# Performance work log

Measured on AMD Instinct MI355X. Metric: run time of the kernel, lower is better.

Reference implementation:

```python
import jax, jax.numpy as jnp
import numpy as np

B, IN, OUT, H = 32768, 512, 512, 8
DH = OUT // H
SCALE = float(np.sqrt(DH))


def setup_inputs() -> dict:
    key = jax.random.key(0)
    ks = jax.random.split(key, 10)
    inp = {
        "protein_features": jax.random.normal(ks[0], (B, IN), jnp.float32),
        "ligand_features": jax.random.normal(ks[1], (B, IN), jnp.float32),
    }
    names = ["q1", "k1", "v1", "q2", "k2", "v2", "o1", "o2"]
    for i, n in enumerate(names):
        fan_in = IN if n[0] in "qkv" else OUT
        kw, kb = jax.random.split(ks[2 + i])
        inp[f"W{n}"] = jax.random.normal(kw, (OUT, fan_in), jnp.float32) * 0.02
        inp[f"b{n}"] = jax.random.normal(kb, (OUT,), jnp.float32) * 0.02
    return inp


def _attend(q, k, v):
    # q,k,v: [B, 1, H, DH]. Original code does matmul(q, k.transpose(-2,-1))
    # WITHOUT moving heads to a batch axis, so attention mixes the H heads
    # of each sample: scores [B, 1, H, H], softmax over last axis.
    scores = jnp.einsum('bshd,bsed->bshe', q, k) / SCALE
    attn = jax.nn.softmax(scores, axis=-1)
    return jnp.einsum('bshe,bsed->bshd', attn, v)  # [B,1,H,DH]


def reference(protein_features, ligand_features,
              Wq1, bq1, Wk1, bk1, Wv1, bv1,
              Wq2, bq2, Wk2, bk2, Wv2, bv2,
              Wo1, bo1, Wo2, bo2):
    Bn = protein_features.shape[0]

    def proj(x, W, b):  # torch Linear: x @ W^T + b, then view(B, -1, H, DH)
        return (x @ W.T + b).reshape(Bn, -1, H, DH)

    q1 = proj(protein_features, Wq1, bq1)
    k1 = proj(ligand_features, Wk1, bk1)
    v1 = proj(ligand_features, Wv1, bv1)
    q2 = proj(ligand_features, Wq2, bq2)
    k2 = proj(protein_features, Wk2, bk2)
    v2 = proj(protein_features, Wv2, bv2)

    out1 = _attend(q1, k1, v1).reshape(Bn, -1)  # [B, OUT]
    out2 = _attend(q2, k2, v2).reshape(Bn, -1)  # [B, OUT]
    protein_output = out1 @ Wo1.T + bo1
    ligand_output = out2 @ Wo2.T + bo2
    return (protein_output, ligand_output)
```

## Files before the change

kernel.cpp:

```cpp
#include <hip/hip_runtime.h>
#include <hip/hip_bf16.h>

#define B_ROWS 32768
#define K_DIM  512
#define NP     1536

typedef __attribute__((ext_vector_type(8))) short          bf16x8;
typedef __attribute__((ext_vector_type(8))) unsigned short u16x8;
typedef __attribute__((ext_vector_type(4))) unsigned short u16x4;
typedef __attribute__((ext_vector_type(4))) float          f32x4;

static __device__ __forceinline__ unsigned short f2bf(float f) {
  __hip_bfloat16 h = __float2bfloat16(f);
  unsigned short u; __builtin_memcpy(&u, &h, 2); return u;
}
static __device__ __forceinline__ float bf2f(unsigned short u) {
  unsigned int x = ((unsigned int)u) << 16; float f; __builtin_memcpy(&f, &x, 4); return f;
}

static __device__ __forceinline__ void gload_lds16(const void* g, void* l) {
  __builtin_amdgcn_global_load_lds(
      (const __attribute__((address_space(1))) void*)g,
      (__attribute__((address_space(3))) void*)l, 16, 0, 0);
}

__global__ __launch_bounds__(256) void pack_kernel(
    const float* __restrict__ Wq1, const float* __restrict__ Wk1,
    const float* __restrict__ Wv1, const float* __restrict__ Wq2,
    const float* __restrict__ Wk2, const float* __restrict__ Wv2,
    const float* __restrict__ Wo1, const float* __restrict__ Wo2,
    const float* __restrict__ bq1, const float* __restrict__ bk1,
    const float* __restrict__ bv1, const float* __restrict__ bq2,
    const float* __restrict__ bk2, const float* __restrict__ bv2,
    unsigned short* __restrict__ Wp, unsigned short* __restrict__ Wl,
    unsigned short* __restrict__ Wo1b, unsigned short* __restrict__ Wo2b,
    float* __restrict__ bp, float* __restrict__ bl)
{
  const int gid = blockIdx.x * 256 + threadIdx.x;
  const int idx = gid * 4;
  const float* src; unsigned short* dst;
  if (idx < 786432) {
    int n = idx >> 9, k = idx & 511;
    const float* W = (n < 512) ? (Wq1 + (size_t)n * 512)
                   : (n < 1024) ? (Wk2 + (size_t)(n - 512) * 512)
                                : (Wv2 + (size_t)(n - 1024) * 512);
    src = W + k; dst = Wp + idx;
  } else if (idx < 1572864) {
    int r = idx - 786432; int n = r >> 9, k = r & 511;
    const float* W = (n < 512) ? (Wk1 + (size_t)n * 512)
                   : (n < 1024) ? (Wv1 + (size_t)(n - 512) * 512)
                                : (Wq2 + (size_t)(n - 1024) * 512);
    src = W + k; dst = Wl + r;
  } else if (idx < 1835008) {
    int r = idx - 1572864; src = Wo1 + r; dst = Wo1b + r;
  } else {
    int r = idx - 1835008; src = Wo2 + r; dst = Wo2b + r;
  }
  float4 v = *reinterpret_cast<const float4*>(src);
  u16x4 o; o[0] = f2bf(v.x); o[1] = f2bf(v.y); o[2] = f2bf(v.z); o[3] = f2bf(v.w);
  *reinterpret_cast<u16x4*>(dst) = o;

  if (gid < 1536) {
    int n = gid;
    bp[n] = (n < 512) ? bq1[n] : (n < 1024) ? bk2[n - 512] : bv2[n - 1024];
  } else if (gid < 3072) {
    int n = gid - 1536;
    bl[n] = (n < 512) ? bk1[n] : (n < 1024) ? bv1[n - 512] : bq2[n - 1024];
  }
}

__global__ __launch_bounds__(256) void cvt_kernel(
    const float* __restrict__ xp, const float* __restrict__ xl,
    unsigned short* __restrict__ xpb, unsigned short* __restrict__ xlb)
{
  const size_t gid = (size_t)blockIdx.x * 256 + threadIdx.x;
  size_t i = gid * 8;
  const float* src; unsigned short* dst;
  if (i < 16777216) { src = xp + i; dst = xpb + i; }
  else              { src = xl + (i - 16777216); dst = xlb + (i - 16777216); }
  float4 a = ((const float4*)src)[0];
  float4 b = ((const float4*)src)[1];
  u16x8 o;
  o[0] = f2bf(a.x); o[1] = f2bf(a.y); o[2] = f2bf(a.z); o[3] = f2bf(a.w);
  o[4] = f2bf(b.x); o[5] = f2bf(b.y); o[6] = f2bf(b.z); o[7] = f2bf(b.w);
  *(u16x8*)dst = o;
}

template<bool OUT_F32>
__global__ __launch_bounds__(512, 2)
void gemm8p(const unsigned short* __restrict__ Aptr, int lda,
            const unsigned short* __restrict__ Wb,
            const float* __restrict__ bias,
            void* __restrict__ Cptr, int ldc, int ntiles)
{
  extern __shared__ __align__(16) unsigned short lds[];
  const int SLOT = 24576, BOFF = 16384;

  const int nwg = gridDim.x, cpx = nwg >> 3, b0 = blockIdx.x;
  const int wk = (b0 & 7) * cpx + (b0 >> 3);
  const int mt = wk / ntiles, nt = wk - mt * ntiles;
  const int m0 = mt << 8, n0 = nt << 7;

  const int tid = threadIdx.x;
  const int lane = tid & 63, w = tid >> 6;
  const int wm = w >> 1, wn = w & 1;
  const int fr = lane & 15, fk = lane >> 4, frx = fr & 7;

  const int r8 = tid >> 3;
  const int k8 = (tid & 7) ^ (r8 & 7);
  const unsigned short* Ab = Aptr + (size_t)(m0 + r8) * lda + k8 * 8;
  const unsigned short* Bb = Wb  + (size_t)(n0 + r8) * 512 + k8 * 8;
  const int ldsW = w * 512;

  const int koff0 = ((0 + fk) ^ frx) * 8;
  const int koff1 = ((4 + fk) ^ frx) * 8;

  f32x4 acc[4][4] = {};

#define STAGE_A(kt, s, j) \
  gload_lds16(Ab + (size_t)(kt) * 64 + (size_t)(j) * 64 * lda, \
              &lds[(s) * SLOT + (j) * 4096 + ldsW])
#define STAGE_B(kt, s, j) \
  gload_lds16(Bb + (size_t)(kt) * 64 + (size_t)(j) * 64 * 512, \
              &lds[(s) * SLOT + BOFF + (j) * 4096 + ldsW])

  STAGE_A(0, 0, 0); STAGE_A(0, 0, 1); STAGE_A(0, 0, 2); STAGE_A(0, 0, 3);
  STAGE_B(0, 0, 0); STAGE_B(0, 0, 1);
  STAGE_A(1, 1, 0); STAGE_A(1, 1, 1); STAGE_A(1, 1, 2); STAGE_A(1, 1, 3);
  STAGE_B(1, 1, 0); STAGE_B(1, 1, 1);
  asm volatile("s_waitcnt vmcnt(6)" ::: "memory");
  __builtin_amdgcn_s_barrier();

  int rd = 0;
  for (int t = 0; t < 8; ++t) {
    const int As_ = rd * SLOT, Bs_ = rd * SLOT + BOFF;
    const int st  = rd ? rd - 1 : 2;
    const bool pre = (t < 6);

    bf16x8 bfr[4][2], afq[2][2];
#pragma unroll
    for (int ni = 0; ni < 4; ++ni) {
      const int rb = Bs_ + (wn * 64 + ni * 16 + fr) * 64;
      bfr[ni][0] = *(const bf16x8*)&lds[rb + koff0];
      bfr[ni][1] = *(const bf16x8*)&lds[rb + koff1];
    }
#pragma unroll
    for (int m2 = 0; m2 < 2; ++m2) {
      const int ra = As_ + (wm * 64 + m2 * 16 + fr) * 64;
      afq[m2][0] = *(const bf16x8*)&lds[ra + koff0];
      afq[m2][1] = *(const bf16x8*)&lds[ra + koff1];
    }
    if (pre) { STAGE_A(t + 2, st, 0); STAGE_A(t + 2, st, 1); STAGE_A(t + 2, st, 2); }
    asm volatile("s_waitcnt lgkmcnt(8)" ::: "memory");
    __builtin_amdgcn_s_barrier();
    asm volatile("s_waitcnt lgkmcnt(0)" ::: "memory");
    __builtin_amdgcn_sched_barrier(0);
    __builtin_amdgcn_s_setprio(1);
#pragma unroll
    for (int m2 = 0; m2 < 2; ++m2)
#pragma unroll
      for (int ni = 0; ni < 4; ++ni)
#pragma unroll
        for (int kc = 0; kc < 2; ++kc)
          acc[m2][ni] = __builtin_amdgcn_mfma_f32_16x16x32_bf16(
              afq[m2][kc], bfr[ni][kc], acc[m2][ni], 0, 0, 0);
    __builtin_amdgcn_s_setprio(0);
    __builtin_amdgcn_s_barrier();

#pragma unroll
    for (int m2 = 0; m2 < 2; ++m2) {
      const int ra = As_ + (wm * 64 + 32 + m2 * 16 + fr) * 64;
      afq[m2][0] = *(const bf16x8*)&lds[ra + koff0];
      afq[m2][1] = *(const bf16x8*)&lds[ra + koff1];
    }
    if (pre) { STAGE_A(t + 2, st, 3); STAGE_B(t + 2, st, 0); STAGE_B(t + 2, st, 1); }
    if (pre)            asm volatile("s_waitcnt vmcnt(6)" ::: "memory");
    else if (t == 6)    asm volatile("s_waitcnt vmcnt(0)" ::: "memory");
    __builtin_amdgcn_s_barrier();
    asm volatile("s_waitcnt lgkmcnt(0)" ::: "memory");
    __builtin_amdgcn_sched_barrier(0);
    __builtin_amdgcn_s_setprio(1);
#pragma unroll
    for (int m2 = 0; m2 < 2; ++m2)
#pragma unroll
      for (int ni = 0; ni < 4; ++ni)
#pragma unroll
        for (int kc = 0; kc < 2; ++kc)
          acc[2 + m2][ni] = __builtin_amdgcn_mfma_f32_16x16x32_bf16(
              afq[m2][kc], bfr[ni][kc], acc[2 + m2][ni], 0, 0, 0);
    __builtin_amdgcn_s_setprio(0);
    __builtin_amdgcn_s_barrier();

    rd = (rd + 1 == 3) ? 0 : rd + 1;
  }
#undef STAGE_A
#undef STAGE_B

#pragma unroll
  for (int ni = 0; ni < 4; ++ni) {
    const int col = n0 + wn * 64 + ni * 16 + fr;
    const float bv = bias[col];
#pragma unroll
    for (int mi = 0; mi < 4; ++mi) {
      const int rbase = m0 + wm * 64 + mi * 16 + fk * 4;
#pragma unroll
      for (int j = 0; j < 4; ++j) {
        const float v = acc[mi][ni][j] + bv;
        if (OUT_F32)
          ((float*)Cptr)[(size_t)(rbase + j) * ldc + col] = v;
        else
          ((unsigned short*)Cptr)[(size_t)(rbase + j) * ldc + col] = f2bf(v);
      }
    }
  }
}

__global__ __launch_bounds__(256, 4)
void attn_kernel(unsigned short* __restrict__ qkvp, unsigned short* __restrict__ qkvl)
{
  __shared__ float lds[4][1696];
  const int w = threadIdx.x >> 6, lane = threadIdx.x & 63;
  const size_t r = (size_t)blockIdx.x * 4 + w;
  unsigned short* rp = qkvp + r * NP;
  unsigned short* rl = qkvl + r * NP;
  const int l8 = lane * 8;

  u16x8 q1 = *(const u16x8*)(rp + l8);
  u16x8 k2 = *(const u16x8*)(rp + 512 + l8);
  u16x8 v2 = *(const u16x8*)(rp + 1024 + l8);
  u16x8 k1 = *(const u16x8*)(rl + l8);
  u16x8 v1 = *(const u16x8*)(rl + 512 + l8);
  u16x8 q2 = *(const u16x8*)(rl + 1024 + l8);

  float* Q   = &lds[w][0];
  float* Kk  = Q + 544;
  float* V   = Kk + 544;
  float* ATT = V + 544;
  const int h = lane >> 3, e = lane & 7;
  const int sb = h * 68 + (lane & 7) * 8;

  auto stage = [&](u16x8 qv, u16x8 kv, u16x8 vv) {
#pragma unroll
    for (int j = 0; j < 8; ++j) {
      Q [sb + j] = bf2f((unsigned short)qv[j]);
      Kk[sb + j] = bf2f((unsigned short)kv[j]);
      V [sb + j] = bf2f((unsigned short)vv[j]);
    }
  };
  auto attend = [&](unsigned short* outp) {
    float s = 0.f;
#pragma unroll
    for (int d = 0; d < 64; ++d) s += Q[h * 68 + d] * Kk[e * 68 + d];
    s *= 0.125f;
    float m = fmaxf(s, __shfl_xor(s, 1, 8));
    m = fmaxf(m, __shfl_xor(m, 2, 8));
    m = fmaxf(m, __shfl_xor(m, 4, 8));
    const float p = __expf(s - m);
    float su = p;
    su += __shfl_xor(su, 1, 8); su += __shfl_xor(su, 2, 8); su += __shfl_xor(su, 4, 8);
    ATT[lane] = p / su;
    float o[8];
    const int d0 = (lane & 7) * 8;
#pragma unroll
    for (int j = 0; j < 8; ++j) {
      float a = 0.f;
#pragma unroll
      for (int e2 = 0; e2 < 8; ++e2) a += ATT[h * 8 + e2] * V[e2 * 68 + d0 + j];
      o[j] = a;
    }
    u16x8 ob;
#pragma unroll
    for (int j = 0; j < 8; ++j) ob[j] = f2bf(o[j]);
    *(u16x8*)(outp + l8) = ob;
  };

  stage(q1, k1, v1);
  attend(rp);
  stage(q2, k2, v2);
  attend(rl);
}

extern "C" void kernel_launch(void* const* d_in, const int* in_sizes, int n_in,
                              void* d_out, int out_size, void* d_ws, size_t ws_size,
                              hipStream_t stream)
{
  const float* xp  = (const float*)d_in[0];
  const float* xl  = (const float*)d_in[1];
  const float* Wq1 = (const float*)d_in[2];   const float* bq1 = (const float*)d_in[3];
  const float* Wk1 = (const float*)d_in[4];   const float* bk1 = (const float*)d_in[5];
  const float* Wv1 = (const float*)d_in[6];   const float* bv1 = (const float*)d_in[7];
  const float* Wq2 = (const float*)d_in[8];   const float* bq2 = (const float*)d_in[9];
  const float* Wk2 = (const float*)d_in[10];  const float* bk2 = (const float*)d_in[11];
  const float* Wv2 = (const float*)d_in[12];  const float* bv2 = (const float*)d_in[13];
  const float* Wo1 = (const float*)d_in[14];  const float* bo1 = (const float*)d_in[15];
  const float* Wo2 = (const float*)d_in[16];  const float* bo2 = (const float*)d_in[17];

  char* p = (char*)d_ws;
  unsigned short* Wp   = (unsigned short*)p; p += (size_t)786432 * 2;
  unsigned short* Wl   = (unsigned short*)p; p += (size_t)786432 * 2;
  unsigned short* Wo1b = (unsigned short*)p; p += (size_t)262144 * 2;
  unsigned short* Wo2b = (unsigned short*)p; p += (size_t)262144 * 2;
  float*          bp   = (float*)p;          p += (size_t)1536 * 4;
  float*          bl   = (float*)p;          p += (size_t)1536 * 4;
  unsigned short* qkvp = (unsigned short*)p; p += (size_t)B_ROWS * NP * 2;
  unsigned short* qkvl = (unsigned short*)p; p += (size_t)B_ROWS * NP * 2;
  (void)ws_size; (void)in_sizes; (void)n_in; (void)out_size;

  unsigned short* xpb = (unsigned short*)d_out;
  unsigned short* xlb = xpb + (size_t)B_ROWS * 512;

  const int LDSB = 147456;
  hipFuncSetAttribute((const void*)gemm8p<false>,
                      hipFuncAttributeMaxDynamicSharedMemorySize, LDSB);
  hipFuncSetAttribute((const void*)gemm8p<true>,
                      hipFuncAttributeMaxDynamicSharedMemorySize, LDSB);

  pack_kernel<<<2048, 256, 0, stream>>>(Wq1, Wk1, Wv1, Wq2, Wk2, Wv2, Wo1, Wo2,
                                        bq1, bk1, bv1, bq2, bk2, bv2,
                                        Wp, Wl, Wo1b, Wo2b, bp, bl);
  cvt_kernel<<<16384, 256, 0, stream>>>(xp, xl, xpb, xlb);

  gemm8p<false><<<1536, 512, LDSB, stream>>>(xpb, 512, Wp, bp, qkvp, NP, 12);
  gemm8p<false><<<1536, 512, LDSB, stream>>>(xlb, 512, Wl, bl, qkvl, NP, 12);

  attn_kernel<<<8192, 256, 0, stream>>>(qkvp, qkvl);

  float* out_p = (float*)d_out;
  float* out_l = out_p + (size_t)B_ROWS * 512;
  gemm8p<true><<<512, 512, LDSB, stream>>>(qkvp, NP, Wo1b, bo1, out_p, 512, 4);
  gemm8p<true><<<512, 512, LDSB, stream>>>(qkvl, NP, Wo2b, bo2, out_l, 512, 4);
}
```

Baseline: 502.5 us.

## Enlarge GEMM tile to 256x256 with double-buffered LDS pipeline

Widens each GEMM workgroup's output tile from 256x128 to 256x256, with 8 waves in a 2x4 layout, each computing 128x64. The three-slot, two-ahead prefetch is replaced by a two-buffer, one-ahead scheme, and grid sizes are halved to match. The goal is more reuse per LDS load and fewer redundant global reads of A. The cost is twice the accumulator registers, shallower prefetch that may expose latency, and fewer workgroups (768 and 256) to fill the CUs.

```diff
diff --git a/kernel.cpp b/kernel.cpp
--- a/kernel.cpp
+++ b/kernel.cpp
@@ -94,17 +94,17 @@
             void* __restrict__ Cptr, int ldc, int ntiles)
 {
   extern __shared__ __align__(16) unsigned short lds[];
-  const int SLOT = 24576, BOFF = 16384;
+  const int BUF = 32768, BOFF = 16384;
 
   const int nwg = gridDim.x, cpx = nwg >> 3, b0 = blockIdx.x;
   const int wk = (b0 & 7) * cpx + (b0 >> 3);
   const int mt = wk / ntiles, nt = wk - mt * ntiles;
-  const int m0 = mt << 8, n0 = nt << 7;
+  const int m0 = mt << 8, n0 = nt << 8;
 
   const int tid = threadIdx.x;
   const int lane = tid & 63, w = tid >> 6;
-  const int wm = w >> 1, wn = w & 1;
-  const int fr = lane & 15, fk = lane >> 4, frx = fr & 7;
+  const int wm = w >> 2, wn = w & 3;
+  const int fr = lane & 15, fk = lane >> 4;
 
   const int r8 = tid >> 3;
   const int k8 = (tid & 7) ^ (r8 & 7);
@@ -112,106 +112,116 @@
   const unsigned short* Bb = Wb  + (size_t)(n0 + r8) * 512 + k8 * 8;
   const int ldsW = w * 512;
 
-  const int koff0 = ((0 + fk) ^ frx) * 8;
-  const int koff1 = ((4 + fk) ^ frx) * 8;
-
-  f32x4 acc[4][4] = {};
-
-#define STAGE_A(kt, s, j) \
-  gload_lds16(Ab + (size_t)(kt) * 64 + (size_t)(j) * 64 * lda, \
-              &lds[(s) * SLOT + (j) * 4096 + ldsW])
-#define STAGE_B(kt, s, j) \
-  gload_lds16(Bb + (size_t)(kt) * 64 + (size_t)(j) * 64 * 512, \
-              &lds[(s) * SLOT + BOFF + (j) * 4096 + ldsW])
-
-  STAGE_A(0, 0, 0); STAGE_A(0, 0, 1); STAGE_A(0, 0, 2); STAGE_A(0, 0, 3);
+  const int koff0 = ((0 + fk) ^ (fr & 7)) * 8;
+  const int koff1 = ((4 + fk) ^ (fr & 7)) * 8;
+
+  f32x4 acc[8][4] = {};
+
+#define STAGE_A(kt, bf, hf) do { \
+    gload_lds16(Ab + (size_t)((hf) * 128) * lda + (kt) * 64, \
+                &lds[(bf) * BUF + ((hf) * 128) * 64 + ldsW]); \
+    gload_lds16(Ab + (size_t)((hf) * 128 + 64) * lda + (kt) * 64, \
+                &lds[(bf) * BUF + ((hf) * 128 + 64) * 64 + ldsW]); } while (0)
+#define STAGE_B(kt, bf, hf) do { \
+    gload_lds16(Bb + (size_t)((hf) * 128) * 512 + (kt) * 64, \
+                &lds[(bf) * BUF + BOFF + ((hf) * 128) * 64 + ldsW]); \
+    gload_lds16(Bb + (size_t)((hf) * 128 + 64) * 512 + (kt) * 64, \
+                &lds[(bf) * BUF + BOFF + ((hf) * 128 + 64) * 64 + ldsW]); } while (0)
+
+#define MFMA16(base) \
+  _Pragma("unroll") \
+  for (int mi = 0; mi < 4; ++mi) \
+    _Pragma("unroll") \
+    for (int ni = 0; ni < 4; ++ni) \
+      acc[(base) + mi][ni] = __builtin_amdgcn_mfma_f32_16x16x32_bf16( \
+          af[mi], bq[ni], acc[(base) + mi][ni], 0, 0, 0)
+
+  STAGE_A(0, 0, 0); STAGE_A(0, 0, 1);
   STAGE_B(0, 0, 0); STAGE_B(0, 0, 1);
-  STAGE_A(1, 1, 0); STAGE_A(1, 1, 1); STAGE_A(1, 1, 2); STAGE_A(1, 1, 3);
-  STAGE_B(1, 1, 0); STAGE_B(1, 1, 1);
-  asm volatile("s_waitcnt vmcnt(6)" ::: "memory");
+  asm volatile("s_waitcnt vmcnt(0)" ::: "memory");
   __builtin_amdgcn_s_barrier();
 
-  int rd = 0;
   for (int t = 0; t < 8; ++t) {
-    const int As_ = rd * SLOT, Bs_ = rd * SLOT + BOFF;
-    const int st  = rd ? rd - 1 : 2;
-    const bool pre = (t < 6);
-
-    bf16x8 bfr[4][2], afq[2][2];
-#pragma unroll
-    for (int ni = 0; ni < 4; ++ni) {
-      const int rb = Bs_ + (wn * 64 + ni * 16 + fr) * 64;
-      bfr[ni][0] = *(const bf16x8*)&lds[rb + koff0];
-      bfr[ni][1] = *(const bf16x8*)&lds[rb + koff1];
-    }
-#pragma unroll
-    for (int m2 = 0; m2 < 2; ++m2) {
-      const int ra = As_ + (wm * 64 + m2 * 16 + fr) * 64;
-      afq[m2][0] = *(const bf16x8*)&lds[ra + koff0];
-      afq[m2][1] = *(const bf16x8*)&lds[ra + koff1];
-    }
-    if (pre) { STAGE_A(t + 2, st, 0); STAGE_A(t + 2, st, 1); STAGE_A(t + 2, st, 2); }
-    asm volatile("s_waitcnt lgkmcnt(8)" ::: "memory");
+    const int R = t & 1, W = 1 - R;
+    const int Ard = R * BUF, Brd = R * BUF + BOFF;
+    const bool pre = (t < 7);
+    bf16x8 bq[4], af[4];
+
+#pragma unroll
+    for (int ni = 0; ni < 4; ++ni)
+      bq[ni] = *(const bf16x8*)&lds[Brd + (wn * 64 + ni * 16 + fr) * 64 + koff0];
+#pragma unroll
+    for (int mi = 0; mi < 4; ++mi)
+      af[mi] = *(const bf16x8*)&lds[Ard + (wm * 128 + mi * 16 + fr) * 64 + koff0];
+    if (pre) { STAGE_A(t + 1, W, 0); STAGE_A(t + 1, W, 1); }
     __builtin_amdgcn_s_barrier();
     asm volatile("s_waitcnt lgkmcnt(0)" ::: "memory");
     __builtin_amdgcn_sched_barrier(0);
     __builtin_amdgcn_s_setprio(1);
-#pragma unroll
-    for (int m2 = 0; m2 < 2; ++m2)
-#pragma unroll
-      for (int ni = 0; ni < 4; ++ni)
-#pragma unroll
-        for (int kc = 0; kc < 2; ++kc)
-          acc[m2][ni] = __builtin_amdgcn_mfma_f32_16x16x32_bf16(
-              afq[m2][kc], bfr[ni][kc], acc[m2][ni], 0, 0, 0);
+    MFMA16(0);
     __builtin_amdgcn_s_setprio(0);
     __builtin_amdgcn_s_barrier();
 
 #pragma unroll
-    for (int m2 = 0; m2 < 2; ++m2) {
-      const int ra = As_ + (wm * 64 + 32 + m2 * 16 + fr) * 64;
-      afq[m2][0] = *(const bf16x8*)&lds[ra + koff0];
-      afq[m2][1] = *(const bf16x8*)&lds[ra + koff1];
-    }
-    if (pre) { STAGE_A(t + 2, st, 3); STAGE_B(t + 2, st, 0); STAGE_B(t + 2, st, 1); }
-    if (pre)            asm volatile("s_waitcnt vmcnt(6)" ::: "memory");
-    else if (t == 6)    asm volatile("s_waitcnt vmcnt(0)" ::: "memory");
+    for (int mi = 0; mi < 4; ++mi)
+      af[mi] = *(const bf16x8*)&lds[Ard + (wm * 128 + 64 + mi * 16 + fr) * 64 + koff0];
+    if (pre) { STAGE_B(t + 1, W, 0); STAGE_B(t + 1, W, 1); }
     __builtin_amdgcn_s_barrier();
     asm volatile("s_waitcnt lgkmcnt(0)" ::: "memory");
     __builtin_amdgcn_sched_barrier(0);
     __builtin_amdgcn_s_setprio(1);
-#pragma unroll
-    for (int m2 = 0; m2 < 2; ++m2)
-#pragma unroll
-      for (int ni = 0; ni < 4; ++ni)
-#pragma unroll
-        for (int kc = 0; kc < 2; ++kc)
-          acc[2 + m2][ni] = __builtin_amdgcn_mfma_f32_16x16x32_bf16(
-              afq[m2][kc], bfr[ni][kc], acc[2 + m2][ni], 0, 0, 0);
+    MFMA16(4);
     __builtin_amdgcn_s_setprio(0);
     __builtin_amdgcn_s_barrier();
 
-    rd = (rd + 1 == 3) ? 0 : rd + 1;
+#pragma unroll
+    for (int ni = 0; ni < 4; ++ni)
+      bq[ni] = *(const bf16x8*)&lds[Brd + (wn * 64 + ni * 16 + fr) * 64 + koff1];
+#pragma unroll
+    for (int mi = 0; mi < 4; ++mi)
+      af[mi] = *(const bf16x8*)&lds[Ard + (wm * 128 + mi * 16 + fr) * 64 + koff1];
+    __builtin_amdgcn_s_barrier();
+    asm volatile("s_waitcnt lgkmcnt(0)" ::: "memory");
+    __builtin_amdgcn_sched_barrier(0);
+    __builtin_amdgcn_s_setprio(1);
+    MFMA16(0);
+    __builtin_amdgcn_s_setprio(0);
+    __builtin_amdgcn_s_barrier();
+
+#pragma unroll
+    for (int mi = 0; mi < 4; ++mi)
+      af[mi] = *(const bf16x8*)&lds[Ard + (wm * 128 + 64 + mi * 16 + fr) * 64 + koff1];
+    if (pre) asm volatile("s_waitcnt vmcnt(0)" ::: "memory");
+    __builtin_amdgcn_s_barrier();
+    asm volatile("s_waitcnt lgkmcnt(0)" ::: "memory");
+    __builtin_amdgcn_sched_barrier(0);
+    __builtin_amdgcn_s_setprio(1);
+    MFMA16(4);
+    __builtin_amdgcn_s_setprio(0);
+    __builtin_amdgcn_s_barrier();
   }
 #undef STAGE_A
 #undef STAGE_B
+#undef MFMA16
 
 #pragma unroll
   for (int ni = 0; ni < 4; ++ni) {
     const int col = n0 + wn * 64 + ni * 16 + fr;
     const float bv = bias[col];
 #pragma unroll
-    for (int mi = 0; mi < 4; ++mi) {
-      const int rbase = m0 + wm * 64 + mi * 16 + fk * 4;
-#pragma unroll
-      for (int j = 0; j < 4; ++j) {
-        const float v = acc[mi][ni][j] + bv;
-        if (OUT_F32)
-          ((float*)Cptr)[(size_t)(rbase + j) * ldc + col] = v;
-        else
-          ((unsigned short*)Cptr)[(size_t)(rbase + j) * ldc + col] = f2bf(v);
+    for (int mh = 0; mh < 2; ++mh)
+#pragma unroll
+      for (int mi = 0; mi < 4; ++mi) {
+        const int rbase = m0 + wm * 128 + mh * 64 + mi * 16 + fk * 4;
+#pragma unroll
+        for (int j = 0; j < 4; ++j) {
+          const float v = acc[mh * 4 + mi][ni][j] + bv;
+          if (OUT_F32)
+            ((float*)Cptr)[(size_t)(rbase + j) * ldc + col] = v;
+          else
+            ((unsigned short*)Cptr)[(size_t)(rbase + j) * ldc + col] = f2bf(v);
+        }
       }
-    }
   }
 }
 
@@ -309,7 +319,7 @@
   unsigned short* xpb = (unsigned short*)d_out;
   unsigned short* xlb = xpb + (size_t)B_ROWS * 512;
 
-  const int LDSB = 147456;
+  const int LDSB = 131072;
   hipFuncSetAttribute((const void*)gemm8p<false>,
                       hipFuncAttributeMaxDynamicSharedMemorySize, LDSB);
   hipFuncSetAttribute((const void*)gemm8p<true>,
@@ -320,13 +330,13 @@
                                         Wp, Wl, Wo1b, Wo2b, bp, bl);
   cvt_kernel<<<16384, 256, 0, stream>>>(xp, xl, xpb, xlb);
 
-  gemm8p<false><<<1536, 512, LDSB, stream>>>(xpb, 512, Wp, bp, qkvp, NP, 12);
-  gemm8p<false><<<1536, 512, LDSB, stream>>>(xlb, 512, Wl, bl, qkvl, NP, 12);
+  gemm8p<false><<<768, 512, LDSB, stream>>>(xpb, 512, Wp, bp, qkvp, NP, 6);
+  gemm8p<false><<<768, 512, LDSB, stream>>>(xlb, 512, Wl, bl, qkvl, NP, 6);
 
   attn_kernel<<<8192, 256, 0, stream>>>(qkvp, qkvl);
 
   float* out_p = (float*)d_out;
   float* out_l = out_p + (size_t)B_ROWS * 512;
-  gemm8p<true><<<512, 512, LDSB, stream>>>(qkvp, NP, Wo1b, bo1, out_p, 512, 4);
-  gemm8p<true><<<512, 512, LDSB, stream>>>(qkvl, NP, Wo2b, bo2, out_l, 512, 4);
-}
+  gemm8p<true><<<256, 512, LDSB, stream>>>(qkvp, NP, Wo1b, bo1, out_p, 512, 2);
+  gemm8p<true><<<256, 512, LDSB, stream>>>(qkvl, NP, Wo2b, bo2, out_l, 512, 2);
+}
```

New measurement: 537.5 us. +7.0%, slower.
